# Performance work log

Hardware: AMD Instinct MI355X
Metric: run time of the kernel (lower is better)

## Reference

```python
import jax, jax.numpy as jnp
import numpy as np

C = 2048      # in_dim (fixed by Incidence_matrix conv)
P = 8         # patch_size
HW = 64       # feature_size
BN_EPS = 1e-5


def setup_inputs() -> dict:
    key = jax.random.key(0)
    ks = jax.random.split(key, 12)
    B = 4
    x = jax.random.normal(ks[0], (B, C, HW, HW), dtype=jnp.float32)
    s = 0.02
    Wk = jax.random.normal(ks[1], (C // 8, C), dtype=jnp.float32) * s
    bk = jax.random.normal(ks[2], (C // 8,), dtype=jnp.float32) * s
    Wq = jax.random.normal(ks[3], (C // 8, C), dtype=jnp.float32) * s
    bq = jax.random.normal(ks[4], (C // 8,), dtype=jnp.float32) * s
    Wv = jax.random.normal(ks[5], (C, C), dtype=jnp.float32) * s
    bv = jax.random.normal(ks[6], (C,), dtype=jnp.float32) * s
    inc_W = jax.random.normal(ks[7], (256, C), dtype=jnp.float32) * s
    inc_b = jax.random.normal(ks[8], (256,), dtype=jnp.float32) * s
    bn_gamma = jnp.ones((256,), dtype=jnp.float32)
    bn_beta = jnp.zeros((256,), dtype=jnp.float32)
    bn_mean = jax.random.normal(ks[9], (256,), dtype=jnp.float32) * 0.1
    bn_var = jax.random.uniform(ks[10], (256,), dtype=jnp.float32) + 0.5
    return {"x": x, "Wk": Wk, "bk": bk, "Wq": Wq, "bq": bq, "Wv": Wv,
            "bv": bv, "inc_W": inc_W, "inc_b": inc_b, "bn_gamma": bn_gamma,
            "bn_beta": bn_beta, "bn_mean": bn_mean, "bn_var": bn_var}


def _forward(x, Wk, bk, Wq, bq, Wv, bv, inc_W, inc_b, bn_gamma, bn_beta, bn_mean, bn_var):
    B, Cc, H, W = x.shape
    nh, nw = H // P, W // P
    N = nh * nw
    Ck = Cc // 8

    # Incidence branch: 1x1 conv -> BN (eval) -> ReLU
    inc = jnp.einsum('bchw,kc->bkhw', x, inc_W) + inc_b[:, None, None]
    inc = (inc - bn_mean[:, None, None]) * (bn_gamma[:, None, None]
          / jnp.sqrt(bn_var[:, None, None] + BN_EPS)) + bn_beta[:, None, None]
    inc = jax.nn.relu(inc)
    # 4x4 avg/max pool (stride 4), then relu each and add
    inc5 = inc.reshape(B, 256, H // 4, 4, W // 4, 4)
    inc_pool = jax.nn.relu(inc5.mean((3, 5))) + jax.nn.relu(inc5.max((3, 5)))
    inc_flat = inc_pool.reshape(B, 256, -1)[:, :, :N]          # [B,256,N] (only first N cols used)

    # Patchify exactly as torch: rearrange 'b c (h p1)(w p2) -> b (h w)(p1 p2 c)'
    # then each flat (p1 p2 c) vector is reinterpreted (view) as (C,p,p).
    patches = (x.reshape(B, Cc, nh, P, nw, P)
                 .transpose(0, 2, 4, 3, 5, 1)                  # [B,nh,nw,p,p,C]
                 .reshape(B, N, Cc, P, P))                      # faithful scrambled view

    # Shared 1x1 KQV projections over all patches
    K = jnp.einsum('bncpq,kc->bnkpq', patches, Wk) + bk[:, None, None]   # [B,N,C/8,p,p]
    Q = jnp.einsum('bncpq,kc->bnkpq', patches, Wq) + bq[:, None, None]
    V = jnp.einsum('bncpq,kc->bnkpq', patches, Wv) + bv[:, None, None]   # [B,N,C,p,p]

    # Q_block = sum_i Q_i * incidence scalar per channel
    Q_block = jnp.einsum('bnkpq,bkn->bkpq', Q, inc_flat)        # [B,C/8,p,p]

    Jp = Q_block.reshape(B, Ck, P * P).transpose(0, 2, 1)        # [B,p2,C/8]
    Kp = K.reshape(B, N, Ck, P * P)                              # [B,N,C/8,p2]
    scores = jnp.einsum('bxc,bncy->bnxy', Jp, Kp)                # [B,N,p2,p2]
    A = jax.nn.softmax(scores, axis=2)                           # torch softmax dim=1
    Vp = V.reshape(B, N, Cc, P * P)                              # [B,N,C,p2]
    out = jnp.einsum('bncx,bnxy->bncy', Vp, A)                   # [B,N,C,p2]

    # cat along height then view back to [B,C,H,W] (faithful scrambled reshape)
    out = out.transpose(0, 2, 1, 3).reshape(B, Cc, H, W)
    return out + x


def reference(x, Wk, bk, Wq, bq, Wv, bv, inc_W, inc_b, bn_gamma, bn_beta, bn_mean, bn_var):
    return _forward(x, Wk, bk, Wq, bq, Wv, bv, inc_W, inc_b,
                    bn_gamma, bn_beta, bn_mean, bn_var)
```

## Files before the change

kernel.cpp:

```cpp
#include <hip/hip_runtime.h>
#include <cstdint>
#include <cstddef>


typedef _Float16 f16_t;
typedef __attribute__((ext_vector_type(8))) _Float16 f16x8;
typedef __attribute__((ext_vector_type(4))) _Float16 f16x4;
typedef __attribute__((ext_vector_type(4))) float f32x4;

#define GLD16(gsrc, ldst) __builtin_amdgcn_global_load_lds( \
    (__attribute__((address_space(1))) void*)(gsrc),        \
    (__attribute__((address_space(3))) void*)(ldst), 16, 0, 0)

__device__ __forceinline__ void split16(float v, f16_t& h, f16_t& l) {
  h = (f16_t)v;
  l = (f16_t)(v - (float)h);
}

__global__ __launch_bounds__(256)
void prep_kernel(const float* __restrict__ Wk, const float* __restrict__ bk,
                 const float* __restrict__ Wq, const float* __restrict__ bq,
                 const float* __restrict__ Wv, const float* __restrict__ incW,
                 f16_t* __restrict__ Wkq_a0, f16_t* __restrict__ Wkq_a1,
                 f16_t* __restrict__ Wv_f,
                 f16_t* __restrict__ incW_a0, f16_t* __restrict__ incW_a1,
                 float* __restrict__ bias_kq)
{
  __shared__ float lds[2048];
  const int row = blockIdx.x;
  const int t = threadIdx.x;
  const float* src;
  f16_t* d0;
  f16_t* d1;
  bool permute = true;
  if (row < 256) {
    src = Wk + (size_t)row * 2048; d0 = Wkq_a0 + (size_t)row * 2048; d1 = Wkq_a1 + (size_t)row * 2048;
  } else if (row < 512) {
    src = Wq + (size_t)(row - 256) * 2048; d0 = Wkq_a0 + (size_t)row * 2048; d1 = Wkq_a1 + (size_t)row * 2048;
  } else if (row < 2560) {
    src = Wv + (size_t)(row - 512) * 2048; d0 = Wv_f + (size_t)(row - 512) * 2048; d1 = nullptr;
  } else {
    src = incW + (size_t)(row - 2560) * 2048; d0 = incW_a0 + (size_t)(row - 2560) * 2048;
    d1 = incW_a1 + (size_t)(row - 2560) * 2048; permute = false;
  }
#pragma unroll
  for (int i = 0; i < 8; ++i) lds[i * 256 + t] = src[i * 256 + t];
  if (row < 512 && t == 0) bias_kq[row] = (row < 256) ? bk[row] : bq[row - 256];
  __syncthreads();
#pragma unroll
  for (int i = 0; i < 8; ++i) {
    int kh = i * 256 + t;
    int cp = permute ? (((kh >> 3) & 7) * 256 + (kh & 7) * 32 + (kh >> 6)) : kh;
    float v = lds[cp];
    f16_t hh, ll;
    split16(v, hh, ll);
    d0[kh] = hh;
    if (d1) d1[kh] = ll;
  }
}

__global__ __launch_bounds__(256)
void gather_kernel(const float* __restrict__ x,
                   f16_t* __restrict__ P0, f16_t* __restrict__ P1)
{
  const int bid = blockIdx.x;
  const int b = bid >> 7;
  const int ph = (bid >> 4) & 7;
  const int cc = bid & 15;
  const int t = threadIdx.x;
  const int pix = t & 127;
  const int p1 = pix >> 4, p2q = pix & 15;
  const int w = p2q * 4;
  const int pw = w >> 3, p2 = w & 7;
  const size_t patch = (size_t)(b * 64 + ph * 8 + pw);
  for (int it = 0; it < 64; ++it) {
    int cl = it * 2 + (t >> 7);
    int c = cc * 128 + cl;
    int j = c & 63, tq = c >> 6;
    const float4 v = *(const float4*)&x[(((size_t)b * 2048 + c) * 64 + ph * 8 + p1) * 64 + w];
    size_t dst = patch * 131072 + (size_t)j * 2048 + tq * 64 + p1 * 8 + p2;
    float vv[4] = {v.x, v.y, v.z, v.w};
    f16x4 h, l;
#pragma unroll
    for (int u = 0; u < 4; ++u) {
      f16_t hh, ll;
      split16(vv[u], hh, ll);
      h[u] = hh; l[u] = ll;
    }
    *(f16x4*)&P0[dst] = h;
    *(f16x4*)&P1[dst] = l;
  }
}

__global__ __launch_bounds__(256)
void xt_kernel(const float* __restrict__ x,
               f16_t* __restrict__ T0, f16_t* __restrict__ T1)
{
  __shared__ float lds[64][65];
  const int bid = blockIdx.x;
  const int b = bid >> 9;
  const int h = (bid >> 5) & 15;
  const int cc = bid & 31;
  const int t = threadIdx.x;
  {
    int ci = t >> 2, w4 = t & 3;
    const float* src = &x[(((size_t)b * 2048 + cc * 64 + ci) * 64 + h) * 64];
#pragma unroll
    for (int it = 0; it < 4; ++it) {
      int w0 = it * 16 + w4 * 4;
      const float4 v = *(const float4*)&src[w0];
      lds[ci][w0 + 0] = v.x; lds[ci][w0 + 1] = v.y;
      lds[ci][w0 + 2] = v.z; lds[ci][w0 + 3] = v.w;
    }
  }
  __syncthreads();
  const int w = t >> 2, cq = t & 3;
  const size_t rowbase = ((size_t)b * 1024 + h * 64 + w) * 2048 + cc * 64 + cq * 16;
  f16x8 H0, H1, L0, L1;
#pragma unroll
  for (int u = 0; u < 8; ++u) {
    f16_t hh, ll;
    split16(lds[cq * 16 + u][w], hh, ll);
    H0[u] = hh; L0[u] = ll;
  }
#pragma unroll
  for (int u = 0; u < 8; ++u) {
    f16_t hh, ll;
    split16(lds[cq * 16 + 8 + u][w], hh, ll);
    H1[u] = hh; L1[u] = ll;
  }
  *(f16x8*)&T0[rowbase] = H0; *(f16x8*)&T0[rowbase + 8] = H1;
  *(f16x8*)&T1[rowbase] = L0; *(f16x8*)&T1[rowbase + 8] = L1;
}

template<int PHASES, int EPI, int SLICES>
__global__ __launch_bounds__(256)
void gemm_kernel(const f16_t* __restrict__ A0, const f16_t* __restrict__ A1,
                 const f16_t* __restrict__ B0, const f16_t* __restrict__ B1,
                 float* __restrict__ Cf, f16_t* __restrict__ Cb,
                 const float* __restrict__ bias, int MB, int ldc)
{
  __shared__ f16_t As[128 * 64];
  __shared__ f16_t Bs[128 * 64];
  const int nwg = gridDim.x;
  const int q = nwg >> 3;
  const int bid = ((int)blockIdx.x & 7) * q + ((int)blockIdx.x >> 3);
  const int tiles = nwg / SLICES;
  const int slice = bid / tiles;
  const int rem = bid % tiles;
  const int nb = rem / MB, mb = rem % MB;
  const int m0 = mb * 128, n0 = nb * 128;
  const int t = threadIdx.x;
  const int lane = t & 63, wv = t >> 6;
  const int wm = (wv >> 1) * 64, wn = (wv & 1) * 64;
  const int l15 = lane & 15, l4 = lane >> 4;

  const f32x4 vzero = {0.f, 0.f, 0.f, 0.f};
  f32x4 acc[4][4];
#pragma unroll
  for (int i = 0; i < 4; ++i)
#pragma unroll
    for (int j = 0; j < 4; ++j) acc[i][j] = vzero;

  constexpr int LOCAL = (32 * PHASES) / SLICES;
  for (int s = 0; s < LOCAL; ++s) {
    const int step = slice * LOCAL + s;
    const int ph = step >> 5;
    const int k0 = (step & 31) << 6;
    const f16_t* Ab = (PHASES == 3 && ph == 2) ? A1 : A0;
    const f16_t* Bb = (PHASES == 3 && ph == 1) ? B1 : B0;
    __syncthreads();
#pragma unroll
    for (int i = 0; i < 4; ++i) {
      int e = i * 2048 + t * 8;
      int row = e >> 6;
      int gl = ((e >> 3) & 7) ^ (row & 7);
      GLD16(Ab + (size_t)(m0 + row) * 2048 + k0 + gl * 8, &As[e]);
    }
#pragma unroll
    for (int i = 0; i < 4; ++i) {
      int e = i * 2048 + t * 8;
      int row = e >> 6;
      int gl = ((e >> 3) & 7) ^ (row & 7);
      GLD16(Bb + (size_t)(n0 + row) * 2048 + k0 + gl * 8, &Bs[e]);
    }
    __syncthreads();
#pragma unroll
    for (int ks = 0; ks < 2; ++ks) {
      f16x8 a[4], bb[4];
#pragma unroll
      for (int i = 0; i < 4; ++i) {
        int r = wm + i * 16 + l15;
        int g = (ks * 4 + l4) ^ (r & 7);
        a[i] = *(const f16x8*)&As[r * 64 + g * 8];
      }
#pragma unroll
      for (int j = 0; j < 4; ++j) {
        int r = wn + j * 16 + l15;
        int g = (ks * 4 + l4) ^ (r & 7);
        bb[j] = *(const f16x8*)&Bs[r * 64 + g * 8];
      }
#pragma unroll
      for (int i = 0; i < 4; ++i)
#pragma unroll
        for (int j = 0; j < 4; ++j)
          acc[i][j] = __builtin_amdgcn_mfma_f32_16x16x32_f16(a[i], bb[j], acc[i][j], 0, 0, 0);
    }
  }

  float* Cp = (EPI == 0) ? Cf + (size_t)slice * (size_t)MB * 128 * (size_t)ldc : nullptr;
#pragma unroll
  for (int i = 0; i < 4; ++i) {
#pragma unroll
    for (int j = 0; j < 4; ++j) {
      int nloc = n0 + wn + j * 16 + l15;
#pragma unroll
      for (int r = 0; r < 4; ++r) {
        int m = m0 + wm + i * 16 + l4 * 4 + r;
        float bsv = (SLICES == 1 || slice == 0) ? bias[m] : 0.f;
        float v = acc[i][j][r] + bsv;
        if (EPI == 0) {
          Cp[(size_t)m * ldc + nloc] = v;
        } else {
          int patch = nloc >> 6, jj = nloc & 63;
          Cb[(size_t)patch * 131072 + (size_t)m * 64 + jj] = (f16_t)v;
        }
      }
    }
  }
}

__global__ void pool_kernel(const float* __restrict__ incout,
                            const float* __restrict__ bnmean, const float* __restrict__ bnvar,
                            const float* __restrict__ gamma, const float* __restrict__ beta,
                            float* __restrict__ incf)
{
  const int blk = blockIdx.x;
  const int b = blk >> 8, k = blk & 255;
  const int n = threadIdx.x;
  const int r = n >> 4, cq = n & 15;
  const float sc = gamma[k] * rsqrtf(bnvar[k] + 1e-5f);
  const float sh = beta[k] - bnmean[k] * sc;
  const size_t PSTR = (size_t)256 * 4096;
  const size_t base = (size_t)k * 4096 + b * 1024 + (r * 4) * 64 + cq * 4;
  float sum = 0.f, mx = 0.f;
#pragma unroll
  for (int dr = 0; dr < 4; ++dr)
#pragma unroll
    for (int dw = 0; dw < 4; ++dw) {
      size_t idx = base + dr * 64 + dw;
      float raw = incout[idx] + incout[idx + PSTR] + incout[idx + 2 * PSTR];
      float v = fmaxf(raw * sc + sh, 0.f);
      sum += v; mx = fmaxf(mx, v);
    }
  incf[(size_t)blk * 64 + n] = sum * (1.f / 16.f) + mx;
}

__global__ void qblock_kernel(const float* __restrict__ KQ,
                              const float* __restrict__ incf,
                              float* __restrict__ Qb)
{
  const int blk = blockIdx.x;
  const int b = blk >> 8, k = blk & 255;
  const int x = threadIdx.x;
  const float* qrow = KQ + (size_t)(256 + k) * 16384 + (size_t)b * 4096;
  const float* ivec = incf + (size_t)blk * 64;
  float a0 = 0.f, a1 = 0.f, a2 = 0.f, a3 = 0.f;
#pragma unroll
  for (int n = 0; n < 16; ++n) {
    a0 += qrow[n * 64 + x] * ivec[n];
    a1 += qrow[(n + 16) * 64 + x] * ivec[n + 16];
    a2 += qrow[(n + 32) * 64 + x] * ivec[n + 32];
    a3 += qrow[(n + 48) * 64 + x] * ivec[n + 48];
  }
  Qb[(size_t)blk * 64 + x] = (a0 + a1) + (a2 + a3);
}

__global__ __launch_bounds__(256)
void scores_kernel(const float* __restrict__ KQ, const float* __restrict__ Qb,
                   f16_t* __restrict__ Asm)
{
  __shared__ float Qs[64 * 64];
  __shared__ float Ks[64 * 64];
  const int pg = blockIdx.x;
  const int b = pg >> 6;
  const int t = threadIdx.x;
  const int y = t >> 2, xg = t & 3;
  float s[16];
#pragma unroll
  for (int i = 0; i < 16; ++i) s[i] = 0.f;
  for (int kc = 0; kc < 4; ++kc) {
    __syncthreads();
#pragma unroll
    for (int i = 0; i < 16; ++i) {
      int idx = i * 256 + t;
      Qs[idx] = Qb[(size_t)b * 16384 + kc * 4096 + idx];
      int kl = idx >> 6, yy = idx & 63;
      Ks[idx] = KQ[(size_t)(kc * 64 + kl) * 16384 + (size_t)pg * 64 + yy];
    }
    __syncthreads();
    float sc[16];
#pragma unroll
    for (int i = 0; i < 16; ++i) sc[i] = 0.f;
    for (int k = 0; k < 64; ++k) {
      float kv = Ks[k * 64 + y];
      const float4* qr = (const float4*)&Qs[k * 64 + xg * 16];
#pragma unroll
      for (int q4 = 0; q4 < 4; ++q4) {
        float4 qv = qr[q4];
        sc[q4 * 4 + 0] += qv.x * kv;
        sc[q4 * 4 + 1] += qv.y * kv;
        sc[q4 * 4 + 2] += qv.z * kv;
        sc[q4 * 4 + 3] += qv.w * kv;
      }
    }
#pragma unroll
    for (int i = 0; i < 16; ++i) s[i] += sc[i];
  }
  float mx = s[0];
#pragma unroll
  for (int i = 1; i < 16; ++i) mx = fmaxf(mx, s[i]);
  mx = fmaxf(mx, __shfl_xor(mx, 1));
  mx = fmaxf(mx, __shfl_xor(mx, 2));
  float p[16], sum = 0.f;
#pragma unroll
  for (int i = 0; i < 16; ++i) { p[i] = expf(s[i] - mx); sum += p[i]; }
  sum += __shfl_xor(sum, 1);
  sum += __shfl_xor(sum, 2);
  const float rinv = 1.f / sum;
#pragma unroll
  for (int i = 0; i < 16; ++i)
    Asm[(size_t)pg * 4096 + y * 64 + xg * 16 + i] = (f16_t)(p[i] * rinv);
}

__global__ __launch_bounds__(256)
void final_kernel(const f16_t* __restrict__ V, const f16_t* __restrict__ Asm,
                  const float* __restrict__ xin, float* __restrict__ out)
{
  __shared__ f16_t Vs[256 * 64];
  __shared__ f16_t Ps[64 * 64];
  const int bid = blockIdx.x;
  const int pg = bid >> 3, cb = bid & 7;
  const int b = pg >> 6, nl = pg & 63;
  const int t = threadIdx.x;
  const int lane = t & 63, wv = t >> 6;
  const int l15 = lane & 15, l4 = lane >> 4;
  const int wm = wv * 64;

#pragma unroll
  for (int i = 0; i < 8; ++i) {
    int e = i * 2048 + t * 8;
    int row = e >> 6;
    int gl = ((e >> 3) & 7) ^ (row & 7);
    GLD16(V + (size_t)pg * 131072 + (size_t)(cb * 256 + row) * 64 + gl * 8, &Vs[e]);
  }
#pragma unroll
  for (int i = 0; i < 2; ++i) {
    int e = i * 2048 + t * 8;
    int row = e >> 6;
    int gl = ((e >> 3) & 7) ^ (row & 7);
    GLD16(Asm + (size_t)pg * 4096 + (size_t)row * 64 + gl * 8, &Ps[e]);
  }
  __syncthreads();

  const f32x4 vzero = {0.f, 0.f, 0.f, 0.f};
  f32x4 acc[4][4];
#pragma unroll
  for (int i = 0; i < 4; ++i)
#pragma unroll
    for (int j = 0; j < 4; ++j) acc[i][j] = vzero;

#pragma unroll
  for (int ks = 0; ks < 2; ++ks) {
    f16x8 a[4], p[4];
#pragma unroll
    for (int i = 0; i < 4; ++i) {
      int r = wm + i * 16 + l15;
      int g = (ks * 4 + l4) ^ (r & 7);
      a[i] = *(const f16x8*)&Vs[r * 64 + g * 8];
    }
#pragma unroll
    for (int j = 0; j < 4; ++j) {
      int r = j * 16 + l15;
      int g = (ks * 4 + l4) ^ (r & 7);
      p[j] = *(const f16x8*)&Ps[r * 64 + g * 8];
    }
#pragma unroll
    for (int i = 0; i < 4; ++i)
#pragma unroll
      for (int j = 0; j < 4; ++j)
        acc[i][j] = __builtin_amdgcn_mfma_f32_16x16x32_f16(a[i], p[j], acc[i][j], 0, 0, 0);
  }

#pragma unroll
  for (int i = 0; i < 4; ++i) {
#pragma unroll
    for (int j = 0; j < 4; ++j) {
      int y = j * 16 + l15;
#pragma unroll
      for (int r = 0; r < 4; ++r) {
        int c = cb * 256 + wm + i * 16 + l4 * 4 + r;
        size_t idx = (((size_t)b * 2048 + c) * 64 + nl) * 64 + y;
        out[idx] = acc[i][j][r] + xin[idx];
      }
    }
  }
}

extern "C" void kernel_launch(void* const* d_in, const int* in_sizes, int n_in,
                              void* d_out, int out_size, void* d_ws, size_t ws_size,
                              hipStream_t stream) {
  const float* x     = (const float*)d_in[0];
  const float* Wk    = (const float*)d_in[1];
  const float* bk    = (const float*)d_in[2];
  const float* Wq    = (const float*)d_in[3];
  const float* bq    = (const float*)d_in[4];
  const float* Wv    = (const float*)d_in[5];
  const float* bv    = (const float*)d_in[6];
  const float* incW  = (const float*)d_in[7];
  const float* incb  = (const float*)d_in[8];
  const float* gamma = (const float*)d_in[9];
  const float* beta  = (const float*)d_in[10];
  const float* bnmean= (const float*)d_in[11];
  const float* bnvar = (const float*)d_in[12];

  char* ws = (char*)d_ws;
  f16_t* Wkq_a0 = (f16_t*)(ws + 0);
  f16_t* Wkq_a1 = (f16_t*)(ws + 2097152);
  f16_t* Wv_f   = (f16_t*)(ws + 4194304);
  f16_t* incW_a0= (f16_t*)(ws + 12582912);
  f16_t* incW_a1= (f16_t*)(ws + 13631488);
  float* biaskq = (float*) (ws + 14680064);
  float* incout = (float*) (ws + 14682112);
  float* incf   = (float*) (ws + 31459328);
  float* Qb     = (float*) (ws + 31721472);
  f16_t* Asm    = (f16_t*)(ws + 31983616);
  float* KQ     = (float*) (ws + 34080768);
  f16_t* xT_a0  = (f16_t*)(ws + 67635200);
  f16_t* xT_a1  = (f16_t*)(ws + 84412416);
  f16_t* P_a0   = (f16_t*)(ws + 101189632);
  f16_t* P_a1   = (f16_t*)(ws + 168298496);
  f16_t* Vbuf   = P_a1;

  prep_kernel<<<2816, 256, 0, stream>>>(Wk, bk, Wq, bq, Wv, incW,
                                        Wkq_a0, Wkq_a1, Wv_f, incW_a0, incW_a1, biaskq);
  gather_kernel<<<512, 256, 0, stream>>>(x, P_a0, P_a1);
  xt_kernel<<<2048, 256, 0, stream>>>(x, xT_a0, xT_a1);
  gemm_kernel<3, 0, 3><<<192, 256, 0, stream>>>(incW_a0, incW_a1, xT_a0, xT_a1,
                                                incout, nullptr, incb, 2, 4096);
  pool_kernel<<<1024, 64, 0, stream>>>(incout, bnmean, bnvar, gamma, beta, incf);
  gemm_kernel<3, 0, 1><<<512, 256, 0, stream>>>(Wkq_a0, Wkq_a1, P_a0, P_a1,
                                                KQ, nullptr, biaskq, 4, 16384);
  qblock_kernel<<<1024, 64, 0, stream>>>(KQ, incf, Qb);
  scores_kernel<<<256, 256, 0, stream>>>(KQ, Qb, Asm);
  gemm_kernel<1, 1, 1><<<2048, 256, 0, stream>>>(Wv_f, Wv_f, P_a0, P_a0,
                                                 nullptr, Vbuf, bv, 16, 64);
  final_kernel<<<2048, 256, 0, stream>>>(Vbuf, Asm, x, (float*)d_out);
}
```

Baseline: 552.4 us.

## Add 256x256-tile GEMM kernel with 8 waves for KQ and V projections

Introduces a new GEMM kernel using 256x256 output tiles, 512 threads, double-buffered direct global-to-LDS loads with XOR swizzle, explicit vmcnt waits and priority hints, plus an XCD-aware block remap. The KQ projection and V projection GEMMs switch to it. The larger tile raises arithmetic intensity and cuts LDS/global traffic per FLOP. In exchange it uses far more registers and LDS, and the smaller grids (128 and 512 blocks) may underfill the GPU's 256 CUs.

```diff
diff --git a/kernel.cpp b/kernel.cpp
--- a/kernel.cpp
+++ b/kernel.cpp
@@ -11,6 +11,11 @@
 #define GLD16(gsrc, ldst) __builtin_amdgcn_global_load_lds( \
     (__attribute__((address_space(1))) void*)(gsrc),        \
     (__attribute__((address_space(3))) void*)(ldst), 16, 0, 0)
+
+#define SBAR() do { __builtin_amdgcn_sched_barrier(0); \
+                    __builtin_amdgcn_s_barrier();      \
+                    __builtin_amdgcn_sched_barrier(0); } while (0)
+#define WVM(N) asm volatile("s_waitcnt vmcnt(" #N ")" ::: "memory")
 
 __device__ __forceinline__ void split16(float v, f16_t& h, f16_t& l) {
   h = (f16_t)v;
@@ -230,6 +235,156 @@
   }
 }
 
+template<int NPH, int EPI, int MBT>
+__global__ __launch_bounds__(512, 2)
+void gemm256_kernel(const f16_t* __restrict__ A0, const f16_t* __restrict__ A1,
+                    const f16_t* __restrict__ B0, const f16_t* __restrict__ B1,
+                    float* __restrict__ Cf, f16_t* __restrict__ Cb,
+                    const float* __restrict__ bias, int ldc)
+{
+  __shared__ f16_t lds[65536];
+  const int nwg = gridDim.x;
+  const int q = nwg >> 3;
+  const int bid = ((int)blockIdx.x & 7) * q + ((int)blockIdx.x >> 3);
+  const int mb = bid % MBT, nb = bid / MBT;
+  const int m0 = mb * 256, n0 = nb * 256;
+  const int t = threadIdx.x;
+  const int lane = t & 63;
+  const int wv = t >> 6;
+  const int wm = wv >> 2;
+  const int wn = wv & 3;
+  const int l15 = lane & 15, l4 = lane >> 4;
+  constexpr int NT = 32 * NPH;
+
+  auto stage = [&](int tt, int op, int kh) {
+    if (tt >= NT) return;
+    const int phse = tt >> 5;
+    const f16_t* src = (op == 0) ? ((NPH == 3 && phse == 2) ? A1 : A0)
+                                 : ((NPH == 3 && phse == 1) ? B1 : B0);
+    const int base0 = (op == 0) ? m0 : n0;
+    const int k0 = ((tt & 31) << 6) + kh * 32;
+    const int rbase = op * 32768 + ((tt & 1) * 2 + kh) * 8192;
+#pragma unroll
+    for (int i = 0; i < 2; ++i) {
+      int e = i * 4096 + t * 8;
+      int r = e >> 5;
+      int s = (e >> 3) & 3;
+      int gs = s ^ (r & 3);
+      GLD16(src + (size_t)(base0 + r) * 2048 + k0 + gs * 8, &lds[rbase + e]);
+    }
+  };
+
+  const f32x4 vzero = {0.f, 0.f, 0.f, 0.f};
+  f32x4 acc[8][4];
+#pragma unroll
+  for (int i = 0; i < 8; ++i)
+#pragma unroll
+    for (int j = 0; j < 4; ++j) acc[i][j] = vzero;
+
+  stage(0, 0, 0); stage(0, 1, 0); stage(0, 0, 1);
+  stage(0, 1, 1); stage(1, 0, 0); stage(1, 1, 0);
+
+  for (int tt = 0; tt < NT; ++tt) {
+    const int buf = tt & 1;
+    const int abase = (buf * 2) * 8192;
+    const int abase1 = (buf * 2 + 1) * 8192;
+    const int bbase = 32768 + (buf * 2) * 8192;
+    const int bbase1 = 32768 + (buf * 2 + 1) * 8192;
+
+    if (tt < NT - 1) { WVM(8); } else { WVM(4); }
+    SBAR();
+    f16x8 b0[4], a[4];
+#pragma unroll
+    for (int j = 0; j < 4; ++j) {
+      int r = wn * 64 + j * 16 + l15;
+      b0[j] = *(const f16x8*)&lds[bbase + r * 32 + (l4 ^ (r & 3)) * 8];
+    }
+#pragma unroll
+    for (int i = 0; i < 4; ++i) {
+      int r = wm * 128 + i * 16 + l15;
+      a[i] = *(const f16x8*)&lds[abase + r * 32 + (l4 ^ (r & 3)) * 8];
+    }
+    stage(tt + 1, 0, 1);
+    __builtin_amdgcn_s_setprio(1);
+#pragma unroll
+    for (int i = 0; i < 4; ++i)
+#pragma unroll
+      for (int j = 0; j < 4; ++j)
+        acc[i][j] = __builtin_amdgcn_mfma_f32_16x16x32_f16(a[i], b0[j], acc[i][j], 0, 0, 0);
+    __builtin_amdgcn_s_setprio(0);
+
+#pragma unroll
+    for (int i = 0; i < 4; ++i) {
+      int r = wm * 128 + 64 + i * 16 + l15;
+      a[i] = *(const f16x8*)&lds[abase + r * 32 + (l4 ^ (r & 3)) * 8];
+    }
+    stage(tt + 1, 1, 1);
+    __builtin_amdgcn_s_setprio(1);
+#pragma unroll
+    for (int i = 0; i < 4; ++i)
+#pragma unroll
+      for (int j = 0; j < 4; ++j)
+        acc[i + 4][j] = __builtin_amdgcn_mfma_f32_16x16x32_f16(a[i], b0[j], acc[i + 4][j], 0, 0, 0);
+    __builtin_amdgcn_s_setprio(0);
+    if (tt < NT - 1) { WVM(8); } else { WVM(0); }
+    SBAR();
+
+    f16x8 b1[4];
+#pragma unroll
+    for (int j = 0; j < 4; ++j) {
+      int r = wn * 64 + j * 16 + l15;
+      b1[j] = *(const f16x8*)&lds[bbase1 + r * 32 + (l4 ^ (r & 3)) * 8];
+    }
+#pragma unroll
+    for (int i = 0; i < 4; ++i) {
+      int r = wm * 128 + i * 16 + l15;
+      a[i] = *(const f16x8*)&lds[abase1 + r * 32 + (l4 ^ (r & 3)) * 8];
+    }
+    stage(tt + 2, 0, 0);
+    __builtin_amdgcn_s_setprio(1);
+#pragma unroll
+    for (int i = 0; i < 4; ++i)
+#pragma unroll
+      for (int j = 0; j < 4; ++j)
+        acc[i][j] = __builtin_amdgcn_mfma_f32_16x16x32_f16(a[i], b1[j], acc[i][j], 0, 0, 0);
+    __builtin_amdgcn_s_setprio(0);
+
+#pragma unroll
+    for (int i = 0; i < 4; ++i) {
+      int r = wm * 128 + 64 + i * 16 + l15;
+      a[i] = *(const f16x8*)&lds[abase1 + r * 32 + (l4 ^ (r & 3)) * 8];
+    }
+    stage(tt + 2, 1, 0);
+    __builtin_amdgcn_s_setprio(1);
+#pragma unroll
+    for (int i = 0; i < 4; ++i)
+#pragma unroll
+      for (int j = 0; j < 4; ++j)
+        acc[i + 4][j] = __builtin_amdgcn_mfma_f32_16x16x32_f16(a[i], b1[j], acc[i + 4][j], 0, 0, 0);
+    __builtin_amdgcn_s_setprio(0);
+    SBAR();
+  }
+
+#pragma unroll
+  for (int i = 0; i < 8; ++i) {
+#pragma unroll
+    for (int j = 0; j < 4; ++j) {
+      int ncol = n0 + wn * 64 + j * 16 + l15;
+#pragma unroll
+      for (int r = 0; r < 4; ++r) {
+        int m = m0 + wm * 128 + i * 16 + l4 * 4 + r;
+        float v = acc[i][j][r] + bias[m];
+        if (EPI == 0) {
+          Cf[(size_t)m * ldc + ncol] = v;
+        } else {
+          int patch = ncol >> 6, jj = ncol & 63;
+          Cb[(size_t)patch * 131072 + (size_t)m * 64 + jj] = (f16_t)v;
+        }
+      }
+    }
+  }
+}
+
 __global__ void pool_kernel(const float* __restrict__ incout,
                             const float* __restrict__ bnmean, const float* __restrict__ bnvar,
                             const float* __restrict__ gamma, const float* __restrict__ beta,
@@ -449,11 +604,11 @@
   gemm_kernel<3, 0, 3><<<192, 256, 0, stream>>>(incW_a0, incW_a1, xT_a0, xT_a1,
                                                 incout, nullptr, incb, 2, 4096);
   pool_kernel<<<1024, 64, 0, stream>>>(incout, bnmean, bnvar, gamma, beta, incf);
-  gemm_kernel<3, 0, 1><<<512, 256, 0, stream>>>(Wkq_a0, Wkq_a1, P_a0, P_a1,
-                                                KQ, nullptr, biaskq, 4, 16384);
+  gemm256_kernel<3, 0, 2><<<128, 512, 0, stream>>>(Wkq_a0, Wkq_a1, P_a0, P_a1,
+                                                   KQ, nullptr, biaskq, 16384);
   qblock_kernel<<<1024, 64, 0, stream>>>(KQ, incf, Qb);
   scores_kernel<<<256, 256, 0, stream>>>(KQ, Qb, Asm);
-  gemm_kernel<1, 1, 1><<<2048, 256, 0, stream>>>(Wv_f, Wv_f, P_a0, P_a0,
-                                                 nullptr, Vbuf, bv, 16, 64);
+  gemm256_kernel<1, 1, 8><<<512, 512, 0, stream>>>(Wv_f, Wv_f, P_a0, P_a0,
+                                                   nullptr, Vbuf, bv, 64);
   final_kernel<<<2048, 256, 0, stream>>>(Vbuf, Asm, x, (float*)d_out);
 }
```

Result: faster. 531.3 us (-3.8%).

## Add multi-buffered async-LDS pipelined GEMM for KQ and V projections

Applied to the files above, without the earlier changes.

Adds a new GEMM kernel with 512-thread workgroups, larger tiles, and a 2- or 3-deep ring of LDS buffers filled by global_load_lds. Explicit vmcnt waits and scheduling barriers let loads for later k-steps overlap MFMA work on the current one. It also swizzles the workgroup order across 8 groups and raises wave priority around the MFMA block. Both the KQ and V projection GEMMs now use it. The aim is to hide global memory latency and reduce the split-K/slice overhead of the old kernel, at the cost of more LDS per workgroup and possibly lower occupancy.

```diff
diff --git a/kernel.cpp b/kernel.cpp
--- a/kernel.cpp
+++ b/kernel.cpp
@@ -11,6 +11,18 @@
 #define GLD16(gsrc, ldst) __builtin_amdgcn_global_load_lds( \
     (__attribute__((address_space(1))) void*)(gsrc),        \
     (__attribute__((address_space(3))) void*)(ldst), 16, 0, 0)
+
+#define SBAR() do { __builtin_amdgcn_sched_barrier(0); \
+                    __builtin_amdgcn_s_barrier();      \
+                    __builtin_amdgcn_sched_barrier(0); } while (0)
+
+template<int N> __device__ __forceinline__ void wvm() {
+  if constexpr (N == 0)       asm volatile("s_waitcnt vmcnt(0)" ::: "memory");
+  else if constexpr (N == 6)  asm volatile("s_waitcnt vmcnt(6)" ::: "memory");
+  else if constexpr (N == 8)  asm volatile("s_waitcnt vmcnt(8)" ::: "memory");
+  else if constexpr (N == 12) asm volatile("s_waitcnt vmcnt(12)" ::: "memory");
+  else if constexpr (N == 16) asm volatile("s_waitcnt vmcnt(16)" ::: "memory");
+}
 
 __device__ __forceinline__ void split16(float v, f16_t& h, f16_t& l) {
   h = (f16_t)v;
@@ -223,6 +235,117 @@
           Cp[(size_t)m * ldc + nloc] = v;
         } else {
           int patch = nloc >> 6, jj = nloc & 63;
+          Cb[(size_t)patch * 131072 + (size_t)m * 64 + jj] = (f16_t)v;
+        }
+      }
+    }
+  }
+}
+
+template<int NPH, int EPI, int MI, int DEPTH, int MBT>
+__global__ __launch_bounds__(512, 2)
+void gemm_pipe_kernel(const f16_t* __restrict__ A0, const f16_t* __restrict__ A1,
+                      const f16_t* __restrict__ B0, const f16_t* __restrict__ B1,
+                      float* __restrict__ Cf, f16_t* __restrict__ Cb,
+                      const float* __restrict__ bias, int ldc)
+{
+  constexpr int BM  = 32 * MI;
+  constexpr int AFP = BM * 64;
+  constexpr int BUF = AFP + 16384;
+  constexpr int LA  = MI / 2;
+  constexpr int L   = LA + 4;
+  constexpr int NT  = 32 * NPH;
+  __shared__ f16_t lds[DEPTH * BUF];
+
+  const int nwg = gridDim.x;
+  const int q = nwg >> 3;
+  const int bid = ((int)blockIdx.x & 7) * q + ((int)blockIdx.x >> 3);
+  const int mb = bid % MBT, nb = bid / MBT;
+  const int m0 = mb * BM, n0 = nb * 256;
+  const int t = threadIdx.x;
+  const int lane = t & 63;
+  const int wv = t >> 6;
+  const int wm = wv >> 2, wn = wv & 3;
+  const int l15 = lane & 15, l4 = lane >> 4;
+
+  auto stage = [&](int tt, int bo) {
+    if (tt >= NT) return;
+    const int ph = tt >> 5;
+    const f16_t* sa = (NPH == 3 && ph == 2) ? A1 : A0;
+    const f16_t* sb = (NPH == 3 && ph == 1) ? B1 : B0;
+    const int k0 = (tt & 31) << 6;
+#pragma unroll
+    for (int i = 0; i < LA; ++i) {
+      int idx = i * 4096 + t * 8;
+      int r = idx >> 6, s = (idx >> 3) & 7, g = s ^ (r & 7);
+      GLD16(sa + (size_t)(m0 + r) * 2048 + k0 + g * 8, &lds[bo + idx]);
+    }
+#pragma unroll
+    for (int i = 0; i < 4; ++i) {
+      int idx = i * 4096 + t * 8;
+      int r = idx >> 6, s = (idx >> 3) & 7, g = s ^ (r & 7);
+      GLD16(sb + (size_t)(n0 + r) * 2048 + k0 + g * 8, &lds[bo + AFP + idx]);
+    }
+  };
+
+  const f32x4 vzero = {0.f, 0.f, 0.f, 0.f};
+  f32x4 acc[MI][4];
+#pragma unroll
+  for (int i = 0; i < MI; ++i)
+#pragma unroll
+    for (int j = 0; j < 4; ++j) acc[i][j] = vzero;
+
+#pragma unroll
+  for (int d = 0; d < DEPTH; ++d) stage(d, d * BUF);
+
+  int bfc = 0, bo = 0;
+  for (int tt = 0; tt < NT; ++tt) {
+    if constexpr (DEPTH == 2) {
+      if (tt < NT - 1) wvm<L>(); else wvm<0>();
+    } else {
+      if (tt < NT - 2) wvm<2 * L>(); else if (tt < NT - 1) wvm<L>(); else wvm<0>();
+    }
+    SBAR();
+#pragma unroll
+    for (int ks = 0; ks < 2; ++ks) {
+      f16x8 a[MI], b[4];
+#pragma unroll
+      for (int j = 0; j < 4; ++j) {
+        int r = wn * 64 + j * 16 + l15;
+        b[j] = *(const f16x8*)&lds[bo + AFP + r * 64 + (((ks * 4 + l4) ^ (r & 7)) * 8)];
+      }
+#pragma unroll
+      for (int i = 0; i < MI; ++i) {
+        int r = wm * (16 * MI) + i * 16 + l15;
+        a[i] = *(const f16x8*)&lds[bo + r * 64 + (((ks * 4 + l4) ^ (r & 7)) * 8)];
+      }
+      __builtin_amdgcn_s_setprio(1);
+#pragma unroll
+      for (int i = 0; i < MI; ++i)
+#pragma unroll
+        for (int j = 0; j < 4; ++j)
+          acc[i][j] = __builtin_amdgcn_mfma_f32_16x16x32_f16(a[i], b[j], acc[i][j], 0, 0, 0);
+      __builtin_amdgcn_s_setprio(0);
+    }
+    SBAR();
+    stage(tt + DEPTH, bo);
+    bfc = (bfc + 1 == DEPTH) ? 0 : bfc + 1;
+    bo = bfc * BUF;
+  }
+
+#pragma unroll
+  for (int i = 0; i < MI; ++i) {
+#pragma unroll
+    for (int j = 0; j < 4; ++j) {
+      int ncol = n0 + wn * 64 + j * 16 + l15;
+#pragma unroll
+      for (int r = 0; r < 4; ++r) {
+        int m = m0 + wm * (16 * MI) + i * 16 + l4 * 4 + r;
+        float v = acc[i][j][r] + bias[m];
+        if (EPI == 0) {
+          Cf[(size_t)m * ldc + ncol] = v;
+        } else {
+          int patch = ncol >> 6, jj = ncol & 63;
           Cb[(size_t)patch * 131072 + (size_t)m * 64 + jj] = (f16_t)v;
         }
       }
@@ -449,11 +572,11 @@
   gemm_kernel<3, 0, 3><<<192, 256, 0, stream>>>(incW_a0, incW_a1, xT_a0, xT_a1,
                                                 incout, nullptr, incb, 2, 4096);
   pool_kernel<<<1024, 64, 0, stream>>>(incout, bnmean, bnvar, gamma, beta, incf);
-  gemm_kernel<3, 0, 1><<<512, 256, 0, stream>>>(Wkq_a0, Wkq_a1, P_a0, P_a1,
-                                                KQ, nullptr, biaskq, 4, 16384);
+  gemm_pipe_kernel<3, 0, 4, 3, 4><<<256, 512, 0, stream>>>(Wkq_a0, Wkq_a1, P_a0, P_a1,
+                                                           KQ, nullptr, biaskq, 16384);
   qblock_kernel<<<1024, 64, 0, stream>>>(KQ, incf, Qb);
   scores_kernel<<<256, 256, 0, stream>>>(KQ, Qb, Asm);
-  gemm_kernel<1, 1, 1><<<2048, 256, 0, stream>>>(Wv_f, Wv_f, P_a0, P_a0,
-                                                 nullptr, Vbuf, bv, 16, 64);
+  gemm_pipe_kernel<1, 1, 8, 2, 8><<<512, 512, 0, stream>>>(Wv_f, Wv_f, P_a0, P_a0,
+                                                           nullptr, Vbuf, bv, 64);
   final_kernel<<<2048, 256, 0, stream>>>(Vbuf, Asm, x, (float*)d_out);
 }
```

Result: faster. 489.2 us (-11.5%).

## Add 8-wave ping-pong GEMM kernel for KQ and V projections

Applied to the files above, without the earlier changes.

Adds a new gemm8 kernel with 512 threads, 256x128 or 256x256 tiles, double-buffered LDS filled by direct global-to-LDS loads with XOR swizzle, and a four-phase schedule. Within each phase it interleaves LDS reads, async prefetch of the next tiles, explicit vmcnt/lgkmcnt waits, barriers and raised-priority MFMA blocks. It also remaps block ids for L2 locality and replaces the split-K style launches of the KQ and V GEMMs with this kernel, dropping the slice logic. The aim is to overlap memory with compute and cut per-tile overhead. In exchange it uses more LDS and registers per block and relies on hand-placed barriers and waits.

```diff
diff --git a/kernel.cpp b/kernel.cpp
--- a/kernel.cpp
+++ b/kernel.cpp
@@ -11,6 +11,22 @@
 #define GLD16(gsrc, ldst) __builtin_amdgcn_global_load_lds( \
     (__attribute__((address_space(1))) void*)(gsrc),        \
     (__attribute__((address_space(3))) void*)(ldst), 16, 0, 0)
+
+#define SBAR() do { __builtin_amdgcn_sched_barrier(0); \
+                    __builtin_amdgcn_s_barrier();      \
+                    __builtin_amdgcn_sched_barrier(0); } while (0)
+
+#define LGKM0() do { asm volatile("s_waitcnt lgkmcnt(0)" ::: "memory"); \
+                     __builtin_amdgcn_sched_barrier(0); } while (0)
+
+template<int N> __device__ __forceinline__ void wvm() {
+  if constexpr (N == 0)       asm volatile("s_waitcnt vmcnt(0)" ::: "memory");
+  else if constexpr (N == 2)  asm volatile("s_waitcnt vmcnt(2)" ::: "memory");
+  else if constexpr (N == 4)  asm volatile("s_waitcnt vmcnt(4)" ::: "memory");
+  else if constexpr (N == 6)  asm volatile("s_waitcnt vmcnt(6)" ::: "memory");
+  else if constexpr (N == 8)  asm volatile("s_waitcnt vmcnt(8)" ::: "memory");
+  __builtin_amdgcn_sched_barrier(0);
+}
 
 __device__ __forceinline__ void split16(float v, f16_t& h, f16_t& l) {
   h = (f16_t)v;
@@ -230,6 +246,138 @@
   }
 }
 
+#define RDA(dst, RH) \
+  _Pragma("unroll") for (int i = 0; i < MIQ; ++i) \
+  _Pragma("unroll") for (int ks = 0; ks < 2; ++ks) { \
+    int r = wm * WTM + (RH) * (WTM / 2) + i * 16 + l15; \
+    dst[i][ks] = *(const f16x8*)&lds[cb + r * 64 + (((ks * 4 + l4) ^ (r & 7)) << 3)]; \
+  }
+#define RDB(dst, CH) \
+  _Pragma("unroll") for (int j = 0; j < NJQ; ++j) \
+  _Pragma("unroll") for (int ks = 0; ks < 2; ++ks) { \
+    int r = wn * WTN + (CH) * (WTN / 2) + j * 16 + l15; \
+    dst[j][ks] = *(const f16x8*)&lds[cb + BBASE + r * 64 + (((ks * 4 + l4) ^ (r & 7)) << 3)]; \
+  }
+#define QMFMA(AR, BR, RH, CH) do { \
+  __builtin_amdgcn_s_setprio(1); \
+  _Pragma("unroll") for (int ks = 0; ks < 2; ++ks) \
+  _Pragma("unroll") for (int i = 0; i < MIQ; ++i) \
+  _Pragma("unroll") for (int j = 0; j < NJQ; ++j) \
+    acc[(RH) * MIQ + i][(CH) * NJQ + j] = __builtin_amdgcn_mfma_f32_16x16x32_f16( \
+        AR[i][ks], BR[j][ks], acc[(RH) * MIQ + i][(CH) * NJQ + j], 0, 0, 0); \
+  __builtin_amdgcn_s_setprio(0); } while (0)
+
+template<int NPH, int EPI, int BM, int BN, int WM, int WN, int MBT>
+__global__ __launch_bounds__(512, 2)
+void gemm8_kernel(const f16_t* __restrict__ A0f, const f16_t* __restrict__ A1f,
+                  const f16_t* __restrict__ B0f, const f16_t* __restrict__ B1f,
+                  float* __restrict__ Cf, f16_t* __restrict__ Cb,
+                  const float* __restrict__ bias, int ldc)
+{
+  constexpr int WTM = BM / WM, WTN = BN / WN;
+  constexpr int MIQ = WTM / 32, NJQ = WTN / 32;
+  constexpr int GA = BM / 128, GB = BN / 128;
+  constexpr int BBASE = BM * 64;
+  constexpr int BUF = (BM + BN) * 64;
+  constexpr int NT = 32 * NPH;
+  constexpr int VW = 2 * GB;
+  __shared__ f16_t lds[2 * BUF];
+
+  const int nwg = gridDim.x;
+  const int q = nwg >> 3;
+  const int bid = ((int)blockIdx.x & 7) * q + ((int)blockIdx.x >> 3);
+  const int mb = bid % MBT, nb = bid / MBT;
+  const int m0 = mb * BM, n0 = nb * BN;
+  const int tid = threadIdx.x;
+  const int lane = tid & 63;
+  const int wv = tid >> 6;
+  const int wm = wv / WN, wn = wv % WN;
+  const int l15 = lane & 15, l4 = lane >> 4;
+
+  auto stageA = [&](int tt, int rg) {
+    if (tt >= NT) return;
+    const f16_t* s = (NPH == 3 && (tt >> 5) == 2) ? A1f : A0f;
+    const int g0 = m0 + rg * (BM / 2);
+    const int base = (tt & 1) * BUF + rg * (BM / 2) * 64;
+    const int k0 = (tt & 31) << 6;
+#pragma unroll
+    for (int i = 0; i < GA; ++i) {
+      int idx = i * 4096 + tid * 8;
+      int r = idx >> 6, sl = (idx >> 3) & 7;
+      GLD16(s + (size_t)(g0 + r) * 2048 + k0 + ((sl ^ (r & 7)) << 3), &lds[base + idx]);
+    }
+  };
+  auto stageB = [&](int tt, int rg) {
+    if (tt >= NT) return;
+    const f16_t* s = (NPH == 3 && (tt >> 5) == 1) ? B1f : B0f;
+    const int g0 = n0 + rg * (BN / 2);
+    const int base = (tt & 1) * BUF + BBASE + rg * (BN / 2) * 64;
+    const int k0 = (tt & 31) << 6;
+#pragma unroll
+    for (int i = 0; i < GB; ++i) {
+      int idx = i * 4096 + tid * 8;
+      int r = idx >> 6, sl = (idx >> 3) & 7;
+      GLD16(s + (size_t)(g0 + r) * 2048 + k0 + ((sl ^ (r & 7)) << 3), &lds[base + idx]);
+    }
+  };
+
+  const f32x4 vzero = {0.f, 0.f, 0.f, 0.f};
+  f32x4 acc[WTM / 16][WTN / 16];
+#pragma unroll
+  for (int i = 0; i < WTM / 16; ++i)
+#pragma unroll
+    for (int j = 0; j < WTN / 16; ++j) acc[i][j] = vzero;
+
+  stageA(0, 0); stageA(0, 1); stageB(0, 0); stageB(0, 1);
+  stageB(1, 0); stageB(1, 1);
+  wvm<VW>();
+  SBAR();
+
+  for (int tt = 0; tt < NT; ++tt) {
+    const int cb = (tt & 1) * BUF;
+    f16x8 a0[MIQ][2], a1[MIQ][2], b0[NJQ][2], b1[NJQ][2];
+    RDA(a0, 0); RDB(b0, 0);
+    stageA(tt + 1, 0);
+    SBAR(); LGKM0();
+    QMFMA(a0, b0, 0, 0);
+    SBAR();
+    RDB(b1, 1);
+    stageA(tt + 1, 1);
+    SBAR(); LGKM0();
+    QMFMA(a0, b1, 0, 1);
+    SBAR();
+    RDA(a1, 1);
+    stageB(tt + 2, 0);
+    SBAR(); LGKM0();
+    QMFMA(a1, b0, 1, 0);
+    SBAR();
+    stageB(tt + 2, 1);
+    if (tt < NT - 2) { wvm<VW>(); } else { wvm<0>(); }
+    SBAR();
+    QMFMA(a1, b1, 1, 1);
+    SBAR();
+  }
+
+#pragma unroll
+  for (int i = 0; i < WTM / 16; ++i) {
+#pragma unroll
+    for (int j = 0; j < WTN / 16; ++j) {
+      int ncol = n0 + wn * WTN + j * 16 + l15;
+#pragma unroll
+      for (int r = 0; r < 4; ++r) {
+        int m = m0 + wm * WTM + i * 16 + l4 * 4 + r;
+        float v = acc[i][j][r] + bias[m];
+        if (EPI == 0) {
+          Cf[(size_t)m * ldc + ncol] = v;
+        } else {
+          int patch = ncol >> 6, jj = ncol & 63;
+          Cb[(size_t)patch * 131072 + (size_t)m * 64 + jj] = (f16_t)v;
+        }
+      }
+    }
+  }
+}
+
 __global__ void pool_kernel(const float* __restrict__ incout,
                             const float* __restrict__ bnmean, const float* __restrict__ bnvar,
                             const float* __restrict__ gamma, const float* __restrict__ beta,
@@ -449,11 +597,11 @@
   gemm_kernel<3, 0, 3><<<192, 256, 0, stream>>>(incW_a0, incW_a1, xT_a0, xT_a1,
                                                 incout, nullptr, incb, 2, 4096);
   pool_kernel<<<1024, 64, 0, stream>>>(incout, bnmean, bnvar, gamma, beta, incf);
-  gemm_kernel<3, 0, 1><<<512, 256, 0, stream>>>(Wkq_a0, Wkq_a1, P_a0, P_a1,
-                                                KQ, nullptr, biaskq, 4, 16384);
+  gemm8_kernel<3, 0, 256, 128, 4, 2, 2><<<256, 512, 0, stream>>>(
+      Wkq_a0, Wkq_a1, P_a0, P_a1, KQ, nullptr, biaskq, 16384);
   qblock_kernel<<<1024, 64, 0, stream>>>(KQ, incf, Qb);
   scores_kernel<<<256, 256, 0, stream>>>(KQ, Qb, Asm);
-  gemm_kernel<1, 1, 1><<<2048, 256, 0, stream>>>(Wv_f, Wv_f, P_a0, P_a0,
-                                                 nullptr, Vbuf, bv, 16, 64);
+  gemm8_kernel<1, 1, 256, 256, 2, 4, 8><<<512, 512, 0, stream>>>(
+      Wv_f, Wv_f, P_a0, P_a0, nullptr, Vbuf, bv, 64);
   final_kernel<<<2048, 256, 0, stream>>>(Vbuf, Asm, x, (float*)d_out);
 }
```

New measurement: 487.0 us. -11.8%, faster.
